# Kernel tuning notes

Measured on AMD Instinct MI355X. Metric: run time of the kernel, lower is better.

Reference implementation:

```python
import jax, jax.numpy as jnp
import numpy as np

N = 50000          # nodes
E = 800000         # directed edges (before self-loops)
F_IN = 256
HIDS = 32
HEADS = 8
N_CLASSES = 40
NEG_SLOPE = 0.2    # PyG GATConv default leaky_relu slope


def setup_inputs() -> dict:
    key = jax.random.key(0)
    ks = jax.random.split(key, 10)
    x = jax.random.normal(ks[0], (N, F_IN), dtype=jnp.float32)
    edge_index = jax.random.randint(ks[1], (2, E), 0, N, dtype=jnp.int32)
    # conv1: F_IN -> HIDS per head, HEADS heads, concat=True
    W1 = jax.random.normal(ks[2], (F_IN, HEADS * HIDS), dtype=jnp.float32) * (1.0 / np.sqrt(F_IN))
    a1_src = jax.random.normal(ks[3], (HEADS, HIDS), dtype=jnp.float32) * 0.1
    a1_dst = jax.random.normal(ks[4], (HEADS, HIDS), dtype=jnp.float32) * 0.1
    b1 = jnp.zeros((HEADS * HIDS,), dtype=jnp.float32)
    # conv2: HEADS*HIDS -> N_CLASSES, 1 head, concat=False
    W2 = jax.random.normal(ks[5], (HEADS * HIDS, N_CLASSES), dtype=jnp.float32) * (1.0 / np.sqrt(HEADS * HIDS))
    a2_src = jax.random.normal(ks[6], (1, N_CLASSES), dtype=jnp.float32) * 0.1
    a2_dst = jax.random.normal(ks[7], (1, N_CLASSES), dtype=jnp.float32) * 0.1
    b2 = jnp.zeros((N_CLASSES,), dtype=jnp.float32)
    return {"x": x, "edge_index": edge_index, "W1": W1, "a1_src": a1_src,
            "a1_dst": a1_dst, "b1": b1, "W2": W2, "a2_src": a2_src,
            "a2_dst": a2_dst, "b2": b2}


def _gat_conv(x, src, dst, W, a_src, a_dst, bias, heads, concat):
    n = x.shape[0]
    c = W.shape[1] // heads
    xw = (x @ W).reshape(n, heads, c)                       # [N,H,C]
    alpha_s = jnp.einsum('nhc,hc->nh', xw, a_src)           # [N,H]
    alpha_d = jnp.einsum('nhc,hc->nh', xw, a_dst)
    e = alpha_s[src] + alpha_d[dst]                         # [Etot,H]
    e = jnp.where(e >= 0, e, NEG_SLOPE * e)                 # leaky_relu
    # segment softmax over incoming edges of each destination node
    m = jax.ops.segment_max(e, dst, num_segments=n)         # [N,H]
    ex = jnp.exp(e - m[dst])
    denom = jax.ops.segment_sum(ex, dst, num_segments=n)    # [N,H]
    alpha = ex / denom[dst]                                 # [Etot,H]
    out = jax.ops.segment_sum(alpha[:, :, None] * xw[src], dst, num_segments=n)  # [N,H,C]
    if concat:
        out = out.reshape(n, heads * c)
    else:
        out = out.mean(axis=1)
    return out + bias


def reference(x, edge_index, W1, a1_src, a1_dst, b1, W2, a2_src, a2_dst, b2):
    n = x.shape[0]
    # add self-loops (PyG GATConv default)
    loop = jnp.arange(n, dtype=edge_index.dtype)
    src = jnp.concatenate([edge_index[0], loop])
    dst = jnp.concatenate([edge_index[1], loop])
    # dropout(p=0.6) layers are identity in eval mode
    h = _gat_conv(x, src, dst, W1, a1_src, a1_dst, b1, HEADS, True)
    h = jax.nn.elu(h)
    out = _gat_conv(h, src, dst, W2, a2_src, a2_dst, b2, 1, False)
    return out
```

## Files before the change

kernel.cpp:

```cpp
#include <hip/hip_runtime.h>
#include <hip/hip_bf16.h>

#define NNODES 50000
#define NPAD   50048
#define NEDGES 800000
#define ETOT   (NEDGES + NNODES)
#define FIN    256
#define HIDS   32
#define HEADS  8
#define NCLS   40
#define NEG    0.2f

#define SCAN_B 256
#define NSCB   ((NNODES + SCAN_B - 1) / SCAN_B)
#define NTILE1 ((NNODES + 63) / 64)

typedef __attribute__((ext_vector_type(8))) short bf16x8;
typedef __attribute__((ext_vector_type(4))) float f32x4;

__device__ __forceinline__ ushort f2bf(float f) {
  unsigned u = __float_as_uint(f);
  unsigned r = (u + 0x7fffu + ((u >> 16) & 1u)) >> 16;
  return (ushort)r;
}
__device__ __forceinline__ float bf2f(ushort u) {
  return __uint_as_float(((unsigned)u) << 16);
}
__device__ __forceinline__ float bflo(unsigned u) { return __uint_as_float(u << 16); }
__device__ __forceinline__ float bfhi(unsigned u) { return __uint_as_float(u & 0xffff0000u); }

__global__ __launch_bounds__(256) void prep_k(
    const float* __restrict__ W1, const float* __restrict__ W2,
    const float* __restrict__ a1src, const float* __restrict__ a1dst,
    const float* __restrict__ a2src, const float* __restrict__ a2dst,
    ushort* __restrict__ w1t, ushort* __restrict__ w2t,
    int* __restrict__ cnt, ushort* __restrict__ hb) {
  int b = blockIdx.x, t = threadIdx.x;
  if (b < 256) {
    int k = b, n = t;
    w1t[(size_t)n * 256 + k] = f2bf(W1[(size_t)k * 256 + n]);
  } else if (b < 272) {
    int j = b - 256, k = t;
    const float* av = (j < 8) ? (a1src + j * 32) : (a1dst + (j - 8) * 32);
    int nb = (j < 8) ? j * 32 : (j - 8) * 32;
    float s = 0.f;
#pragma unroll
    for (int c = 0; c < 32; ++c) s += W1[(size_t)k * 256 + nb + c] * av[c];
    w1t[(size_t)(256 + j) * 256 + k] = f2bf(s);
  } else if (b < 320) {
    w1t[(size_t)b * 256 + t] = 0;
  } else if (b < 384) {
    int n = b - 320, k = t;
    ushort v;
    if (n < NCLS) {
      v = f2bf(W2[(size_t)k * NCLS + n]);
    } else if (n == 40) {
      float s = 0.f;
#pragma unroll
      for (int c = 0; c < NCLS; ++c) s += W2[(size_t)k * NCLS + c] * a2src[c];
      v = f2bf(s);
    } else if (n == 41) {
      float s = 0.f;
#pragma unroll
      for (int c = 0; c < NCLS; ++c) s += W2[(size_t)k * NCLS + c] * a2dst[c];
      v = f2bf(s);
    } else {
      v = 0;
    }
    w2t[(size_t)n * 256 + k] = v;
  } else if (b < 580) {
    int i = (b - 384) * 256 + t;
    if (i < NNODES) cnt[i] = 0;
  } else {
    int r = NNODES + (b - 580);
    hb[(size_t)r * 256 + t] = 0;
  }
}

__global__ __launch_bounds__(256) void gemm1_mfma(
    const float* __restrict__ x, const ushort* __restrict__ w1t,
    ushort* __restrict__ xw1s, float* __restrict__ a1sx, float* __restrict__ a1dx) {
  __shared__ ushort As[64 * 40];
  __shared__ ushort Bs[320 * 40];
  const int tid = threadIdx.x;
  const int m0 = blockIdx.x * 64;
  const int w = tid >> 6, l = tid & 63, lr = l & 15, lq = l >> 4;
  f32x4 acc[4][5];
#pragma unroll
  for (int i = 0; i < 4; ++i)
#pragma unroll
    for (int j = 0; j < 5; ++j) acc[i][j] = (f32x4)0.f;

  for (int k0 = 0; k0 < 256; k0 += 32) {
    {
      int row = tid >> 2, kg = (tid & 3) * 8;
      int gr = m0 + row;
      bf16x8 av;
      if (gr < NNODES) {
        const float4* xp = (const float4*)(x + (size_t)gr * 256 + k0 + kg);
        float4 p0 = xp[0], p1 = xp[1];
        av[0] = (short)f2bf(p0.x); av[1] = (short)f2bf(p0.y);
        av[2] = (short)f2bf(p0.z); av[3] = (short)f2bf(p0.w);
        av[4] = (short)f2bf(p1.x); av[5] = (short)f2bf(p1.y);
        av[6] = (short)f2bf(p1.z); av[7] = (short)f2bf(p1.w);
      } else {
        av = (bf16x8)0;
      }
      *(bf16x8*)&As[row * 40 + kg] = av;
    }
#pragma unroll
    for (int p = 0; p < 5; ++p) {
      int idx = tid + p * 256;
      int n = idx >> 2, kg = (idx & 3) * 8;
      *(bf16x8*)&Bs[n * 40 + kg] = *(const bf16x8*)(w1t + (size_t)n * 256 + k0 + kg);
    }
    __syncthreads();
    bf16x8 af[4], bfr[5];
#pragma unroll
    for (int mt = 0; mt < 4; ++mt)
      af[mt] = *(const bf16x8*)&As[(mt * 16 + lr) * 40 + lq * 8];
#pragma unroll
    for (int nt = 0; nt < 5; ++nt) {
      int tile = nt * 4 + w;
      bfr[nt] = *(const bf16x8*)&Bs[(tile * 16 + lr) * 40 + lq * 8];
    }
#pragma unroll
    for (int mt = 0; mt < 4; ++mt)
#pragma unroll
      for (int nt = 0; nt < 5; ++nt)
        acc[mt][nt] = __builtin_amdgcn_mfma_f32_16x16x32_bf16(af[mt], bfr[nt], acc[mt][nt], 0, 0, 0);
    __syncthreads();
  }
#pragma unroll
  for (int mt = 0; mt < 4; ++mt)
#pragma unroll
    for (int nt = 0; nt < 5; ++nt) {
      int tile = nt * 4 + w;
      if (tile < 16) {
        int colc = tile * 16 + lr;
        int s = colc >> 5, c = colc & 31;
#pragma unroll
        for (int r = 0; r < 4; ++r) {
          int row = m0 + mt * 16 + lq * 4 + r;
          xw1s[((size_t)s * NPAD + row) * 32 + c] = f2bf(acc[mt][nt][r]);
        }
      } else if (tile == 16) {
#pragma unroll
        for (int r = 0; r < 4; ++r) {
          int row = m0 + mt * 16 + lq * 4 + r;
          if (lr < 8) a1sx[(size_t)lr * NPAD + row] = acc[mt][nt][r];
          else        a1dx[(size_t)(lr - 8) * NPAD + row] = acc[mt][nt][r];
        }
      }
    }
}

__global__ __launch_bounds__(256) void gemm2_mfma(
    const ushort* __restrict__ hb, const ushort* __restrict__ w2t,
    ushort* __restrict__ xw2b, float* __restrict__ a2s, float* __restrict__ a2d) {
  const int tid = threadIdx.x;
  const int w = tid >> 6, l = tid & 63, lr = l & 15, lq = l >> 4;
  const int row0 = blockIdx.x * 64 + w * 16;
  f32x4 acc[3];
#pragma unroll
  for (int i = 0; i < 3; ++i) acc[i] = (f32x4)0.f;
#pragma unroll
  for (int ks = 0; ks < 8; ++ks) {
    int k0 = ks * 32;
    bf16x8 af = *(const bf16x8*)(hb + (size_t)(row0 + lr) * 256 + k0 + lq * 8);
#pragma unroll
    for (int nt = 0; nt < 3; ++nt) {
      bf16x8 bfr = *(const bf16x8*)(w2t + (size_t)(nt * 16 + lr) * 256 + k0 + lq * 8);
      acc[nt] = __builtin_amdgcn_mfma_f32_16x16x32_bf16(af, bfr, acc[nt], 0, 0, 0);
    }
  }
#pragma unroll
  for (int nt = 0; nt < 3; ++nt) {
    int colc = nt * 16 + lr;
#pragma unroll
    for (int r = 0; r < 4; ++r) {
      int row = row0 + lq * 4 + r;
      if (colc < NCLS)      xw2b[(size_t)row * 40 + colc] = f2bf(acc[nt][r]);
      else if (colc == 40)  a2s[row] = acc[nt][r];
      else if (colc == 41)  a2d[row] = acc[nt][r];
    }
  }
}

__global__ __launch_bounds__(256) void hist_k(const int* __restrict__ dstA, int* __restrict__ cnt) {
  int e = blockIdx.x * 256 + threadIdx.x;
  if (e >= ETOT) return;
  int d = (e < NEDGES) ? dstA[e] : (e - NEDGES);
  atomicAdd(&cnt[d], 1);
}

__global__ __launch_bounds__(SCAN_B) void scan1_k(const int* __restrict__ deg,
                                                  int* __restrict__ row_ptr,
                                                  int* __restrict__ bsum) {
  __shared__ int sm[SCAN_B];
  int b = blockIdx.x, t = threadIdx.x;
  int idx = b * SCAN_B + t;
  int v = (idx < NNODES) ? deg[idx] : 0;
  sm[t] = v;
  __syncthreads();
#pragma unroll
  for (int off = 1; off < SCAN_B; off <<= 1) {
    int u = (t >= off) ? sm[t - off] : 0;
    __syncthreads();
    sm[t] += u;
    __syncthreads();
  }
  if (idx < NNODES) row_ptr[idx + 1] = sm[t];
  if (t == SCAN_B - 1) bsum[b] = sm[t];
}

__global__ __launch_bounds__(SCAN_B) void scan23_k(const int* __restrict__ bsum,
                                                   int* __restrict__ row_ptr) {
  __shared__ int sm[SCAN_B];
  int b = blockIdx.x, t = threadIdx.x;
  sm[t] = (t < NSCB) ? bsum[t] : 0;
  __syncthreads();
#pragma unroll
  for (int off = 1; off < SCAN_B; off <<= 1) {
    int u = (t >= off) ? sm[t - off] : 0;
    __syncthreads();
    sm[t] += u;
    __syncthreads();
  }
  int offb = (b > 0) ? sm[b - 1] : 0;
  int idx = b * SCAN_B + t;
  if (idx < NNODES) row_ptr[idx + 1] += offb;
  if (b == 0 && t == 0) row_ptr[0] = 0;
}

__global__ __launch_bounds__(256) void scatter_k(const int* __restrict__ srcA, const int* __restrict__ dstA,
                                                 const int* __restrict__ row_ptr, int* __restrict__ cnt,
                                                 int* __restrict__ col) {
  int e = blockIdx.x * 256 + threadIdx.x;
  if (e >= ETOT) return;
  int s, d;
  if (e < NEDGES) { s = srcA[e]; d = dstA[e]; }
  else { s = d = e - NEDGES; }
  int old = atomicSub(&cnt[d], 1);
  col[row_ptr[d] + old - 1] = s;
}

__global__ __launch_bounds__(256) void agg1_k(
    const ushort* __restrict__ xw1s, const float* __restrict__ a1sx, const float* __restrict__ a1dx,
    const int* __restrict__ row_ptr, const int* __restrict__ col,
    const float* __restrict__ b1, ushort* __restrict__ hb) {
  const int b = blockIdx.x;
  const int s = b & 7;
  const int t = threadIdx.x;
  const int node = (b >> 3) * 64 + (t >> 2);
  const int q = t & 3;
  if (node >= NNODES) return;
  const ushort* xs = xw1s + (size_t)s * NPAD * 32 + q * 8;
  const float* as = a1sx + (size_t)s * NPAD;
  const float ad = a1dx[(size_t)s * NPAD + node];
  int i = row_ptr[node];
  const int end = row_ptr[node + 1];
  float den = 0.f;
  float c0 = 0.f, c1 = 0.f, c2 = 0.f, c3 = 0.f, c4 = 0.f, c5 = 0.f, c6 = 0.f, c7 = 0.f;
  for (; i + 2 <= end; i += 2) {
    int s0 = col[i], s1 = col[i + 1];
    uint4 u0 = *(const uint4*)(xs + (size_t)s0 * 32);
    uint4 u1 = *(const uint4*)(xs + (size_t)s1 * 32);
    float e0 = as[s0] + ad;
    float e1 = as[s1] + ad;
    float w0 = __expf(fmaxf(e0, 0.f) + NEG * fminf(e0, 0.f));
    float w1 = __expf(fmaxf(e1, 0.f) + NEG * fminf(e1, 0.f));
    den += w0 + w1;
    c0 += w0 * bflo(u0.x) + w1 * bflo(u1.x);
    c1 += w0 * bfhi(u0.x) + w1 * bfhi(u1.x);
    c2 += w0 * bflo(u0.y) + w1 * bflo(u1.y);
    c3 += w0 * bfhi(u0.y) + w1 * bfhi(u1.y);
    c4 += w0 * bflo(u0.z) + w1 * bflo(u1.z);
    c5 += w0 * bfhi(u0.z) + w1 * bfhi(u1.z);
    c6 += w0 * bflo(u0.w) + w1 * bflo(u1.w);
    c7 += w0 * bfhi(u0.w) + w1 * bfhi(u1.w);
  }
  if (i < end) {
    int s0 = col[i];
    uint4 u0 = *(const uint4*)(xs + (size_t)s0 * 32);
    float e0 = as[s0] + ad;
    float w0 = __expf(fmaxf(e0, 0.f) + NEG * fminf(e0, 0.f));
    den += w0;
    c0 += w0 * bflo(u0.x); c1 += w0 * bfhi(u0.x);
    c2 += w0 * bflo(u0.y); c3 += w0 * bfhi(u0.y);
    c4 += w0 * bflo(u0.z); c5 += w0 * bfhi(u0.z);
    c6 += w0 * bflo(u0.w); c7 += w0 * bfhi(u0.w);
  }
  const float inv = 1.f / den;
  const float4 bv0 = *reinterpret_cast<const float4*>(b1 + s * 32 + q * 8);
  const float4 bv1 = *reinterpret_cast<const float4*>(b1 + s * 32 + q * 8 + 4);
  float o[8];
  o[0] = c0 * inv + bv0.x; o[1] = c1 * inv + bv0.y;
  o[2] = c2 * inv + bv0.z; o[3] = c3 * inv + bv0.w;
  o[4] = c4 * inv + bv1.x; o[5] = c5 * inv + bv1.y;
  o[6] = c6 * inv + bv1.z; o[7] = c7 * inv + bv1.w;
  uint4 pk;
  unsigned r[4];
#pragma unroll
  for (int p = 0; p < 4; ++p) {
    float a = o[2 * p],     va = (a > 0.f) ? a : expm1f(a);
    float c = o[2 * p + 1], vc = (c > 0.f) ? c : expm1f(c);
    r[p] = (unsigned)f2bf(va) | ((unsigned)f2bf(vc) << 16);
  }
  pk.x = r[0]; pk.y = r[1]; pk.z = r[2]; pk.w = r[3];
  *(uint4*)(hb + (size_t)node * 256 + s * 32 + q * 8) = pk;
}

__global__ __launch_bounds__(256) void agg2_k(
    const ushort* __restrict__ xw2b, const float* __restrict__ a2s, const float* __restrict__ a2d,
    const int* __restrict__ row_ptr, const int* __restrict__ col,
    const float* __restrict__ b2, float* __restrict__ out, int n) {
  int wid = (blockIdx.x * 256 + threadIdx.x) >> 6;
  if (wid >= n) return;
  int lane = threadIdx.x & 63;
  int beg = row_ptr[wid], end = row_ptr[wid + 1];
  float ad = a2d[wid];
  float denom = 0.f, acc = 0.f;
  int i = beg;
  for (; i + 4 <= end; i += 4) {
    int s0 = col[i], s1 = col[i + 1], s2 = col[i + 2], s3 = col[i + 3];
    float e0 = a2s[s0] + ad;
    float e1 = a2s[s1] + ad;
    float e2 = a2s[s2] + ad;
    float e3 = a2s[s3] + ad;
    float w0 = __expf(fmaxf(e0, 0.f) + NEG * fminf(e0, 0.f));
    float w1 = __expf(fmaxf(e1, 0.f) + NEG * fminf(e1, 0.f));
    float w2 = __expf(fmaxf(e2, 0.f) + NEG * fminf(e2, 0.f));
    float w3 = __expf(fmaxf(e3, 0.f) + NEG * fminf(e3, 0.f));
    float x0 = 0.f, x1 = 0.f, x2 = 0.f, x3 = 0.f;
    if (lane < NCLS) {
      x0 = bf2f(xw2b[(size_t)s0 * 40 + lane]);
      x1 = bf2f(xw2b[(size_t)s1 * 40 + lane]);
      x2 = bf2f(xw2b[(size_t)s2 * 40 + lane]);
      x3 = bf2f(xw2b[(size_t)s3 * 40 + lane]);
    }
    denom += (w0 + w1) + (w2 + w3);
    acc += w0 * x0 + w1 * x1 + w2 * x2 + w3 * x3;
  }
  for (; i < end; ++i) {
    int s = col[i];
    float e = a2s[s] + ad;
    float w = __expf(fmaxf(e, 0.f) + NEG * fminf(e, 0.f));
    denom += w;
    if (lane < NCLS) acc += w * bf2f(xw2b[(size_t)s * 40 + lane]);
  }
  if (lane < NCLS) out[(size_t)wid * 40 + lane] = acc / denom + b2[lane];
}

extern "C" void kernel_launch(void* const* d_in, const int* in_sizes, int n_in,
                              void* d_out, int out_size, void* d_ws, size_t ws_size,
                              hipStream_t stream) {
  const float* x     = (const float*)d_in[0];
  const int*   ei    = (const int*)d_in[1];
  const float* W1    = (const float*)d_in[2];
  const float* a1src = (const float*)d_in[3];
  const float* a1dst = (const float*)d_in[4];
  const float* b1    = (const float*)d_in[5];
  const float* W2    = (const float*)d_in[6];
  const float* a2src = (const float*)d_in[7];
  const float* a2dst = (const float*)d_in[8];
  const float* b2    = (const float*)d_in[9];
  float* out = (float*)d_out;

  const int* srcA = ei;
  const int* dstA = ei + NEDGES;

  ushort* w1t  = (ushort*)d_ws;
  ushort* w2t  = w1t + (size_t)320 * 256;
  ushort* xw1s = w2t + (size_t)64 * 256;
  ushort* hb   = xw1s + (size_t)NPAD * 256;
  ushort* xw2b = hb + (size_t)NPAD * 256;
  float* a1sx  = (float*)(xw2b + (size_t)NPAD * 40);
  float* a1dx  = a1sx + (size_t)8 * NPAD;
  float* a2s   = a1dx + (size_t)8 * NPAD;
  float* a2d   = a2s + NPAD;
  int* row_ptr = (int*)(a2d + NPAD);
  int* cnt     = row_ptr + (NNODES + 1);
  int* col     = cnt + NNODES;
  int* bsum    = col + ETOT;

  prep_k<<<628, 256, 0, stream>>>(W1, W2, a1src, a1dst, a2src, a2dst, w1t, w2t, cnt, hb);

  gemm1_mfma<<<NPAD / 64, 256, 0, stream>>>(x, w1t, xw1s, a1sx, a1dx);

  hist_k<<<(ETOT + 255) / 256, 256, 0, stream>>>(dstA, cnt);
  scan1_k<<<NSCB, SCAN_B, 0, stream>>>(cnt, row_ptr, bsum);
  scan23_k<<<NSCB, SCAN_B, 0, stream>>>(bsum, row_ptr);
  scatter_k<<<(ETOT + 255) / 256, 256, 0, stream>>>(srcA, dstA, row_ptr, cnt, col);

  agg1_k<<<NTILE1 * 8, 256, 0, stream>>>(xw1s, a1sx, a1dx, row_ptr, col, b1, hb);

  gemm2_mfma<<<NPAD / 64, 256, 0, stream>>>(hb, w2t, xw2b, a2s, a2d);

  agg2_k<<<(NNODES + 3) / 4, 256, 0, stream>>>(xw2b, a2s, a2d, row_ptr, col, b2, out, NNODES);
}
```

Baseline: 258.8 us.

## Sort nodes by in-degree via counting sort to balance agg1 warps

```diff
diff --git a/kernel.cpp b/kernel.cpp
--- a/kernel.cpp
+++ b/kernel.cpp
@@ -34,7 +34,7 @@
     const float* __restrict__ a1src, const float* __restrict__ a1dst,
     const float* __restrict__ a2src, const float* __restrict__ a2dst,
     ushort* __restrict__ w1t, ushort* __restrict__ w2t,
-    int* __restrict__ cnt, ushort* __restrict__ hb) {
+    int* __restrict__ cnt, ushort* __restrict__ hb, int* __restrict__ dbin) {
   int b = blockIdx.x, t = threadIdx.x;
   if (b < 256) {
     int k = b, n = t;
@@ -71,9 +71,11 @@
   } else if (b < 580) {
     int i = (b - 384) * 256 + t;
     if (i < NNODES) cnt[i] = 0;
-  } else {
+  } else if (b < 628) {
     int r = NNODES + (b - 580);
     hb[(size_t)r * 256 + t] = 0;
+  } else {
+    dbin[t] = 0;
   }
 }
 
@@ -196,11 +198,13 @@
 
 __global__ __launch_bounds__(SCAN_B) void scan1_k(const int* __restrict__ deg,
                                                   int* __restrict__ row_ptr,
-                                                  int* __restrict__ bsum) {
+                                                  int* __restrict__ bsum,
+                                                  int* __restrict__ dbin) {
   __shared__ int sm[SCAN_B];
   int b = blockIdx.x, t = threadIdx.x;
   int idx = b * SCAN_B + t;
   int v = (idx < NNODES) ? deg[idx] : 0;
+  if (idx < NNODES) atomicAdd(&dbin[(v < 255) ? v : 255], 1);
   sm[t] = v;
   __syncthreads();
 #pragma unroll
@@ -231,6 +235,32 @@
   int idx = b * SCAN_B + t;
   if (idx < NNODES) row_ptr[idx + 1] += offb;
   if (b == 0 && t == 0) row_ptr[0] = 0;
+}
+
+__global__ __launch_bounds__(256) void binscan_k(int* __restrict__ dbin) {
+  __shared__ int sm[256];
+  int t = threadIdx.x;
+  sm[t] = dbin[t];
+  __syncthreads();
+#pragma unroll
+  for (int off = 1; off < 256; off <<= 1) {
+    int u = (t >= off) ? sm[t - off] : 0;
+    __syncthreads();
+    sm[t] += u;
+    __syncthreads();
+  }
+  dbin[t] = (t > 0) ? sm[t - 1] : 0;
+}
+
+__global__ __launch_bounds__(256) void perm_k(const int* __restrict__ row_ptr,
+                                              int* __restrict__ dbin,
+                                              int* __restrict__ perm) {
+  int n = blockIdx.x * 256 + threadIdx.x;
+  if (n >= NNODES) return;
+  int deg = row_ptr[n + 1] - row_ptr[n];
+  int bin = (deg < 255) ? deg : 255;
+  int pos = atomicAdd(&dbin[bin], 1);
+  perm[pos] = n;
 }
 
 __global__ __launch_bounds__(256) void scatter_k(const int* __restrict__ srcA, const int* __restrict__ dstA,
@@ -247,14 +277,15 @@
 
 __global__ __launch_bounds__(256) void agg1_k(
     const ushort* __restrict__ xw1s, const float* __restrict__ a1sx, const float* __restrict__ a1dx,
-    const int* __restrict__ row_ptr, const int* __restrict__ col,
+    const int* __restrict__ row_ptr, const int* __restrict__ col, const int* __restrict__ perm,
     const float* __restrict__ b1, ushort* __restrict__ hb) {
   const int b = blockIdx.x;
   const int s = b & 7;
   const int t = threadIdx.x;
-  const int node = (b >> 3) * 64 + (t >> 2);
+  const int slot = (b >> 3) * 64 + (t >> 2);
   const int q = t & 3;
-  if (node >= NNODES) return;
+  if (slot >= NNODES) return;
+  const int node = perm[slot];
   const ushort* xs = xw1s + (size_t)s * NPAD * 32 + q * 8;
   const float* as = a1sx + (size_t)s * NPAD;
   const float ad = a1dx[(size_t)s * NPAD + node];
@@ -383,17 +414,21 @@
   int* cnt     = row_ptr + (NNODES + 1);
   int* col     = cnt + NNODES;
   int* bsum    = col + ETOT;
-
-  prep_k<<<628, 256, 0, stream>>>(W1, W2, a1src, a1dst, a2src, a2dst, w1t, w2t, cnt, hb);
+  int* dbin    = bsum + NSCB;
+  int* perm    = dbin + 256;
+
+  prep_k<<<629, 256, 0, stream>>>(W1, W2, a1src, a1dst, a2src, a2dst, w1t, w2t, cnt, hb, dbin);
 
   gemm1_mfma<<<NPAD / 64, 256, 0, stream>>>(x, w1t, xw1s, a1sx, a1dx);
 
   hist_k<<<(ETOT + 255) / 256, 256, 0, stream>>>(dstA, cnt);
-  scan1_k<<<NSCB, SCAN_B, 0, stream>>>(cnt, row_ptr, bsum);
+  scan1_k<<<NSCB, SCAN_B, 0, stream>>>(cnt, row_ptr, bsum, dbin);
   scan23_k<<<NSCB, SCAN_B, 0, stream>>>(bsum, row_ptr);
+  binscan_k<<<1, 256, 0, stream>>>(dbin);
+  perm_k<<<NSCB, 256, 0, stream>>>(row_ptr, dbin, perm);
   scatter_k<<<(ETOT + 255) / 256, 256, 0, stream>>>(srcA, dstA, row_ptr, cnt, col);
 
-  agg1_k<<<NTILE1 * 8, 256, 0, stream>>>(xw1s, a1sx, a1dx, row_ptr, col, b1, hb);
+  agg1_k<<<NTILE1 * 8, 256, 0, stream>>>(xw1s, a1sx, a1dx, row_ptr, col, perm, b1, hb);
 
   gemm2_mfma<<<NPAD / 64, 256, 0, stream>>>(hb, w2t, xw2b, a2s, a2d);
 
```

Measured after the change: 570.2 us. +120.4%, slower.
